# Performance work log

Hardware: AMD Instinct MI355X
Metric: run time of the kernel (lower is better)

The kernel has to match this reference:

```python
import jax, jax.numpy as jnp
import numpy as np

C = 256
POOL = 4

def setup_inputs() -> dict:
    key = jax.random.key(0)
    ks = jax.random.split(key, 8)
    B, H, W = 4, 256, 256
    d = C // 8
    x = jax.random.normal(ks[0], (B, C, H, W), dtype=jnp.float32)
    # 1x1 conv weights stored as [out, in] matrices (kernel_size=1)
    s = 1.0 / np.sqrt(C)
    Wq = jax.random.uniform(ks[1], (d, C), jnp.float32, -s, s)
    bq = jax.random.uniform(ks[2], (d,), jnp.float32, -s, s)
    Wk = jax.random.uniform(ks[3], (d, C), jnp.float32, -s, s)
    bk = jax.random.uniform(ks[4], (d,), jnp.float32, -s, s)
    Wv = jax.random.uniform(ks[5], (C, C), jnp.float32, -s, s)
    bv = jax.random.uniform(ks[6], (C,), jnp.float32, -s, s)
    gamma = jax.random.normal(ks[7], (1,), jnp.float32) * 0.1
    return {"x": x, "Wq": Wq, "bq": bq, "Wk": Wk, "bk": bk,
            "Wv": Wv, "bv": bv, "gamma": gamma}


def reference(x, Wq, bq, Wk, bk, Wv, bv, gamma):
    B, Cc, H, W = x.shape
    Hp, Wp = H // POOL, W // POOL
    # AvgPool2d(kernel=4, stride=4)
    xp = x.reshape(B, Cc, Hp, POOL, Wp, POOL).mean(axis=(3, 5))  # [B,C,Hp,Wp]
    xf = xp.reshape(B, Cc, Hp * Wp)                              # [B,C,N]
    # 1x1 convs == channel matmuls
    q = jnp.einsum('dc,bcn->bdn', Wq, xf) + bq[None, :, None]    # [B,d,N]
    k = jnp.einsum('dc,bcn->bdn', Wk, xf) + bk[None, :, None]    # [B,d,N]
    v = jnp.einsum('ec,bcn->ben', Wv, xf) + bv[None, :, None]    # [B,C,N]
    # energy[b,n,m] = q[:, :, n] . k[:, :, m]
    energy = jnp.einsum('bdn,bdm->bnm', q, k)                    # [B,N,N]
    attn = jax.nn.softmax(energy, axis=-1)
    # out = v @ attn^T  -> out[b,c,n] = sum_m v[b,c,m] * attn[b,n,m]
    out = jnp.einsum('bcm,bnm->bcn', v, attn)                    # [B,C,N]
    out = out.reshape(B, Cc, Hp, Wp)
    # bilinear upsample, half-pixel centers (align_corners=False)
    up = jax.image.resize(out, (B, Cc, H, W), method='bilinear')
    return gamma[0] * up + x
```

## Files before the change

kernel.cpp:

```cpp
#include <hip/hip_runtime.h>

#define B_ 4
#define C_ 256
#define N_ 4096
#define D_ 32

typedef __bf16 bf16;
typedef __bf16 bf16x4 __attribute__((ext_vector_type(4)));
typedef __bf16 bf16x8 __attribute__((ext_vector_type(8)));
typedef float f32x4 __attribute__((ext_vector_type(4)));

__global__ __launch_bounds__(256) void k_prep(
    const float* __restrict__ Wq, const float* __restrict__ bq,
    const float* __restrict__ Wk, const float* __restrict__ bk,
    const float* __restrict__ Wv, const float* __restrict__ bv,
    bf16* __restrict__ wt, float* __restrict__ bias) {
  int r = blockIdx.x, t = threadIdx.x;
  const float* src; float bval;
  if (r < 32)      { src = Wq + (r << 8);        bval = bq[r]; }
  else if (r < 64) { src = Wk + ((r - 32) << 8); bval = bk[r - 32]; }
  else             { src = Wv + ((r - 64) << 8); bval = bv[r - 64]; }
  wt[(r << 8) + t] = (bf16)src[t];
  if (t == 0) bias[r] = bval;
}

__global__ __launch_bounds__(256) void k_fused(const float* __restrict__ x,
    const bf16* __restrict__ wt, const float* __restrict__ bias,
    bf16* __restrict__ qt, bf16* __restrict__ kt, bf16* __restrict__ v) {
  __shared__ bf16 xsb[64][264];
  int tid = threadIdx.x, wave = tid >> 6, l = tid & 63;
  int lg = l >> 4, ll = l & 15;
  int b = blockIdx.x >> 6, hp = blockIdx.x & 63, n0 = hp * 64;

  const float4* x4 = reinterpret_cast<const float4*>(x) +
      ((size_t)((b * 256 + wave * 64) * 256 + hp * 4)) * 64 + l;
  for (int c0 = 0; c0 < 64; c0 += 4) {
    float s[4] = {0.f, 0.f, 0.f, 0.f};
    #pragma unroll
    for (int j = 0; j < 4; ++j) {
      const float4* p = x4 + (size_t)(c0 + j) * 16384;
      #pragma unroll
      for (int dh = 0; dh < 4; ++dh) {
        float4 a = p[dh * 64];
        s[j] += a.x + a.y + a.z + a.w;
      }
    }
    bf16x4 pk;
    #pragma unroll
    for (int j = 0; j < 4; ++j) pk[j] = (bf16)(s[j] * 0.0625f);
    *reinterpret_cast<bf16x4*>(&xsb[l][wave * 64 + c0]) = pk;
  }
  __syncthreads();

  f32x4 acc[5][4];
  #pragma unroll
  for (int j = 0; j < 5; ++j)
    #pragma unroll
    for (int cb = 0; cb < 4; ++cb) acc[j][cb] = (f32x4){0.f, 0.f, 0.f, 0.f};

  for (int kk = 0; kk < 8; ++kk) {
    bf16x8 bfr[4];
    #pragma unroll
    for (int cb = 0; cb < 4; ++cb)
      bfr[cb] = *reinterpret_cast<const bf16x8*>(&xsb[cb * 16 + ll][kk * 32 + lg * 8]);
    #pragma unroll
    for (int j = 0; j < 5; ++j) {
      int rb = wave + j * 4;
      bf16x8 afr = *reinterpret_cast<const bf16x8*>(
          wt + ((size_t)(rb * 16 + ll)) * 256 + kk * 32 + lg * 8);
      #pragma unroll
      for (int cb = 0; cb < 4; ++cb)
        acc[j][cb] = __builtin_amdgcn_mfma_f32_16x16x32_bf16(afr, bfr[cb], acc[j][cb], 0, 0, 0);
    }
  }

  #pragma unroll
  for (int j = 0; j < 5; ++j) {
    int rb = wave + j * 4;
    int row0 = rb * 16 + lg * 4;
    float4 b4 = *reinterpret_cast<const float4*>(bias + row0);
    #pragma unroll
    for (int cb = 0; cb < 4; ++cb) {
      int n = n0 + cb * 16 + ll;
      float v0 = acc[j][cb][0] + b4.x, v1 = acc[j][cb][1] + b4.y;
      float v2 = acc[j][cb][2] + b4.z, v3 = acc[j][cb][3] + b4.w;
      if (row0 < 32) {
        bf16x4 pk = {(bf16)v0, (bf16)v1, (bf16)v2, (bf16)v3};
        *reinterpret_cast<bf16x4*>(qt + ((size_t)(b * N_ + n)) * D_ + row0) = pk;
      } else if (row0 < 64) {
        bf16x4 pk = {(bf16)v0, (bf16)v1, (bf16)v2, (bf16)v3};
        *reinterpret_cast<bf16x4*>(kt + ((size_t)(b * N_ + n)) * D_ + row0 - 32) = pk;
      } else {
        int c = row0 - 64;
        v[((size_t)(b * 256 + c + 0)) * N_ + n] = (bf16)v0;
        v[((size_t)(b * 256 + c + 1)) * N_ + n] = (bf16)v1;
        v[((size_t)(b * 256 + c + 2)) * N_ + n] = (bf16)v2;
        v[((size_t)(b * 256 + c + 3)) * N_ + n] = (bf16)v3;
      }
    }
  }
}

__global__ __launch_bounds__(256) void k_attn(const bf16* __restrict__ qt,
    const bf16* __restrict__ kt, const bf16* __restrict__ v,
    float* __restrict__ outs) {
  __shared__ bf16 p_s[32][264];
  __shared__ float l_stage[4][32];
  __shared__ float l_s[32];
  int tid = threadIdx.x, wave = tid >> 6, l = tid & 63;
  int lg = l >> 4, ll = l & 15;
  int blk = blockIdx.x;
  int b  = (blk & 7) >> 1;
  int nt = ((blk >> 3) << 1) | (blk & 1);
  int n0 = nt * 32;

  const f32x4 fz = {0.f, 0.f, 0.f, 0.f};

  bf16x8 aq[2];
  #pragma unroll
  for (int tnf = 0; tnf < 2; ++tnf)
    aq[tnf] = *reinterpret_cast<const bf16x8*>(
        qt + ((size_t)(b * N_ + n0 + tnf * 16 + ll)) * D_ + lg * 8);

  bf16x8 onesf;
  {
    bf16 o = (bf16)(ll == 0 ? 1.0f : 0.0f);
    #pragma unroll
    for (int e = 0; e < 8; ++e) onesf[e] = o;
  }

  f32x4 acc[2][4];
  f32x4 lacc[2];
  #pragma unroll
  for (int a = 0; a < 2; ++a) {
    lacc[a] = fz;
    #pragma unroll
    for (int cf = 0; cf < 4; ++cf) acc[a][cf] = fz;
  }

  const int mw_off = wave * 64;
  const int cw0    = wave * 64;

  for (int t = 0; t < 16; ++t) {
    int m0 = t * 256;
    #pragma unroll
    for (int tmf = 0; tmf < 4; ++tmf) {
      int mglob = m0 + mw_off + tmf * 16 + ll;
      bf16x8 bk8 = *reinterpret_cast<const bf16x8*>(
          kt + ((size_t)(b * N_ + mglob)) * D_ + lg * 8);
      #pragma unroll
      for (int tnf = 0; tnf < 2; ++tnf) {
        f32x4 e = __builtin_amdgcn_mfma_f32_16x16x32_bf16(aq[tnf], bk8, fz, 0, 0, 0);
        int col = mw_off + tmf * 16 + ll;
        #pragma unroll
        for (int r = 0; r < 4; ++r) {
          float p = __expf(e[r]);
          p_s[tnf * 16 + lg * 4 + r][col] = (bf16)p;
        }
      }
    }
    __syncthreads();
    #pragma unroll
    for (int kk = 0; kk < 8; ++kk) {
      bf16x8 pa[2];
      #pragma unroll
      for (int tnf = 0; tnf < 2; ++tnf)
        pa[tnf] = *reinterpret_cast<const bf16x8*>(
            &p_s[tnf * 16 + ll][kk * 32 + lg * 8]);
      #pragma unroll
      for (int tnf = 0; tnf < 2; ++tnf)
        lacc[tnf] = __builtin_amdgcn_mfma_f32_16x16x32_bf16(pa[tnf], onesf, lacc[tnf], 0, 0, 0);
      #pragma unroll
      for (int cf = 0; cf < 4; ++cf) {
        int c = cw0 + cf * 16 + ll;
        bf16x8 bv8 = *reinterpret_cast<const bf16x8*>(
            v + ((size_t)((b << 8) + c)) * N_ + m0 + kk * 32 + lg * 8);
        acc[0][cf] = __builtin_amdgcn_mfma_f32_16x16x32_bf16(pa[0], bv8, acc[0][cf], 0, 0, 0);
        acc[1][cf] = __builtin_amdgcn_mfma_f32_16x16x32_bf16(pa[1], bv8, acc[1][cf], 0, 0, 0);
      }
    }
    __syncthreads();
  }

  if (ll == 0) {
    #pragma unroll
    for (int tnf = 0; tnf < 2; ++tnf)
      #pragma unroll
      for (int r = 0; r < 4; ++r)
        l_stage[wave][tnf * 16 + lg * 4 + r] = lacc[tnf][r];
  }
  __syncthreads();
  if (tid < 32)
    l_s[tid] = l_stage[0][tid] + l_stage[1][tid] + l_stage[2][tid] + l_stage[3][tid];
  __syncthreads();

  #pragma unroll
  for (int tnf = 0; tnf < 2; ++tnf) {
    #pragma unroll
    for (int r = 0; r < 4; ++r) {
      int tn = tnf * 16 + lg * 4 + r;
      float inv = 1.0f / l_s[tn];
      #pragma unroll
      for (int cf = 0; cf < 4; ++cf) {
        int c = cw0 + cf * 16 + ll;
        outs[((size_t)((b << 8) + c)) * N_ + n0 + tn] = acc[tnf][cf][r] * inv;
      }
    }
  }
}

__global__ __launch_bounds__(256) void k_up(const float* __restrict__ outs,
    const float* __restrict__ x, const float* __restrict__ gamma,
    float* __restrict__ out) {
  int j = blockIdx.x * 256 + threadIdx.x;
  int wq = j & 63, h = (j >> 6) & 255, bc = j >> 14;
  int th = 2 * h - 3;
  int h0 = th < 0 ? -1 : (th >> 3);
  float fh = (float)(th - 8 * h0) * 0.125f;
  int i0h = h0 < 0 ? 0 : h0;
  int i1h = h0 + 1 > 63 ? 63 : h0 + 1;
  const float* s0 = outs + ((size_t)(bc * 64 + i0h)) * 64;
  const float* s1 = outs + ((size_t)(bc * 64 + i1h)) * 64;
  float g = gamma[0];
  float r4[4];
  #pragma unroll
  for (int k2 = 0; k2 < 4; ++k2) {
    int w = wq * 4 + k2;
    int tw = 2 * w - 3;
    int w0 = tw < 0 ? -1 : (tw >> 3);
    float fw = (float)(tw - 8 * w0) * 0.125f;
    int i0 = w0 < 0 ? 0 : w0;
    int i1 = w0 + 1 > 63 ? 63 : w0 + 1;
    float a = s0[i0], bb = s0[i1], cc = s1[i0], dd = s1[i1];
    float top = a + fw * (bb - a);
    float bot = cc + fw * (dd - cc);
    r4[k2] = top + fh * (bot - top);
  }
  size_t o4 = (size_t)(bc * 256 + h) * 64 + wq;
  float4 xv = reinterpret_cast<const float4*>(x)[o4];
  float4 o;
  o.x = g * r4[0] + xv.x; o.y = g * r4[1] + xv.y;
  o.z = g * r4[2] + xv.z; o.w = g * r4[3] + xv.w;
  reinterpret_cast<float4*>(out)[o4] = o;
}

extern "C" void kernel_launch(void* const* d_in, const int* in_sizes, int n_in,
                              void* d_out, int out_size, void* d_ws, size_t ws_size,
                              hipStream_t stream) {
  const float* x     = (const float*)d_in[0];
  const float* Wq    = (const float*)d_in[1];
  const float* bq    = (const float*)d_in[2];
  const float* Wk    = (const float*)d_in[3];
  const float* bk    = (const float*)d_in[4];
  const float* Wv    = (const float*)d_in[5];
  const float* bv    = (const float*)d_in[6];
  const float* gamma = (const float*)d_in[7];
  float* out = (float*)d_out;

  char* ws = (char*)d_ws;
  float* outs = (float*)(ws);
  bf16*  v    = (bf16*) (ws + (16u << 20));
  bf16*  qt   = (bf16*) (ws + (24u << 20));
  bf16*  kt   = (bf16*) (ws + (25u << 20));
  bf16*  wt   = (bf16*) (ws + (26u << 20));
  float* bias = (float*)(ws + (27u << 20));

  hipLaunchKernelGGL(k_prep,  dim3(320),   dim3(256), 0, stream,
                     Wq, bq, Wk, bk, Wv, bv, wt, bias);
  hipLaunchKernelGGL(k_fused, dim3(256),   dim3(256), 0, stream,
                     x, wt, bias, qt, kt, v);
  hipLaunchKernelGGL(k_attn,  dim3(512),   dim3(256), 0, stream, qt, kt, v, outs);
  hipLaunchKernelGGL(k_up,    dim3(65536), dim3(256), 0, stream, outs, x, gamma, out);
}
```

Before: 307.2 us.

## Double threads per block in projection and attention kernels, compute softmax sum in fp32

Both k_fused and k_attn now run 8 waves per block instead of 4, and each wave handles half the channels and keys. This is meant to raise latency hiding with only 256/512 blocks on the device. In k_attn, the row-sum computed by an MFMA against a ones vector is replaced with per-lane fp32 accumulation of exp values followed by shuffle and shared-memory reductions. That removes MFMA work but adds a VALU add per exp. In k_fused, some waves do no work in the last iteration (rb<20), so the load is imbalanced.

After: 298.2 us. -2.9%, faster.

```diff
diff --git a/kernel.cpp b/kernel.cpp
--- a/kernel.cpp
+++ b/kernel.cpp
@@ -24,7 +24,7 @@
   if (t == 0) bias[r] = bval;
 }
 
-__global__ __launch_bounds__(256) void k_fused(const float* __restrict__ x,
+__global__ __launch_bounds__(512) void k_fused(const float* __restrict__ x,
     const bf16* __restrict__ wt, const float* __restrict__ bias,
     bf16* __restrict__ qt, bf16* __restrict__ kt, bf16* __restrict__ v) {
   __shared__ bf16 xsb[64][264];
@@ -33,8 +33,8 @@
   int b = blockIdx.x >> 6, hp = blockIdx.x & 63, n0 = hp * 64;
 
   const float4* x4 = reinterpret_cast<const float4*>(x) +
-      ((size_t)((b * 256 + wave * 64) * 256 + hp * 4)) * 64 + l;
-  for (int c0 = 0; c0 < 64; c0 += 4) {
+      ((size_t)((b * 256 + wave * 32) * 256 + hp * 4)) * 64 + l;
+  for (int c0 = 0; c0 < 32; c0 += 4) {
     float s[4] = {0.f, 0.f, 0.f, 0.f};
     #pragma unroll
     for (int j = 0; j < 4; ++j) {
@@ -48,13 +48,13 @@
     bf16x4 pk;
     #pragma unroll
     for (int j = 0; j < 4; ++j) pk[j] = (bf16)(s[j] * 0.0625f);
-    *reinterpret_cast<bf16x4*>(&xsb[l][wave * 64 + c0]) = pk;
+    *reinterpret_cast<bf16x4*>(&xsb[l][wave * 32 + c0]) = pk;
   }
   __syncthreads();
 
-  f32x4 acc[5][4];
-  #pragma unroll
-  for (int j = 0; j < 5; ++j)
+  f32x4 acc[3][4];
+  #pragma unroll
+  for (int j = 0; j < 3; ++j)
     #pragma unroll
     for (int cb = 0; cb < 4; ++cb) acc[j][cb] = (f32x4){0.f, 0.f, 0.f, 0.f};
 
@@ -64,48 +64,52 @@
     for (int cb = 0; cb < 4; ++cb)
       bfr[cb] = *reinterpret_cast<const bf16x8*>(&xsb[cb * 16 + ll][kk * 32 + lg * 8]);
     #pragma unroll
-    for (int j = 0; j < 5; ++j) {
-      int rb = wave + j * 4;
-      bf16x8 afr = *reinterpret_cast<const bf16x8*>(
-          wt + ((size_t)(rb * 16 + ll)) * 256 + kk * 32 + lg * 8);
-      #pragma unroll
-      for (int cb = 0; cb < 4; ++cb)
-        acc[j][cb] = __builtin_amdgcn_mfma_f32_16x16x32_bf16(afr, bfr[cb], acc[j][cb], 0, 0, 0);
-    }
-  }
-
-  #pragma unroll
-  for (int j = 0; j < 5; ++j) {
-    int rb = wave + j * 4;
-    int row0 = rb * 16 + lg * 4;
-    float4 b4 = *reinterpret_cast<const float4*>(bias + row0);
-    #pragma unroll
-    for (int cb = 0; cb < 4; ++cb) {
-      int n = n0 + cb * 16 + ll;
-      float v0 = acc[j][cb][0] + b4.x, v1 = acc[j][cb][1] + b4.y;
-      float v2 = acc[j][cb][2] + b4.z, v3 = acc[j][cb][3] + b4.w;
-      if (row0 < 32) {
-        bf16x4 pk = {(bf16)v0, (bf16)v1, (bf16)v2, (bf16)v3};
-        *reinterpret_cast<bf16x4*>(qt + ((size_t)(b * N_ + n)) * D_ + row0) = pk;
-      } else if (row0 < 64) {
-        bf16x4 pk = {(bf16)v0, (bf16)v1, (bf16)v2, (bf16)v3};
-        *reinterpret_cast<bf16x4*>(kt + ((size_t)(b * N_ + n)) * D_ + row0 - 32) = pk;
-      } else {
-        int c = row0 - 64;
-        v[((size_t)(b * 256 + c + 0)) * N_ + n] = (bf16)v0;
-        v[((size_t)(b * 256 + c + 1)) * N_ + n] = (bf16)v1;
-        v[((size_t)(b * 256 + c + 2)) * N_ + n] = (bf16)v2;
-        v[((size_t)(b * 256 + c + 3)) * N_ + n] = (bf16)v3;
-      }
-    }
-  }
-}
-
-__global__ __launch_bounds__(256) void k_attn(const bf16* __restrict__ qt,
+    for (int j = 0; j < 3; ++j) {
+      int rb = wave + j * 8;
+      if (rb < 20) {
+        bf16x8 afr = *reinterpret_cast<const bf16x8*>(
+            wt + ((size_t)(rb * 16 + ll)) * 256 + kk * 32 + lg * 8);
+        #pragma unroll
+        for (int cb = 0; cb < 4; ++cb)
+          acc[j][cb] = __builtin_amdgcn_mfma_f32_16x16x32_bf16(afr, bfr[cb], acc[j][cb], 0, 0, 0);
+      }
+    }
+  }
+
+  #pragma unroll
+  for (int j = 0; j < 3; ++j) {
+    int rb = wave + j * 8;
+    if (rb < 20) {
+      int row0 = rb * 16 + lg * 4;
+      float4 b4 = *reinterpret_cast<const float4*>(bias + row0);
+      #pragma unroll
+      for (int cb = 0; cb < 4; ++cb) {
+        int n = n0 + cb * 16 + ll;
+        float v0 = acc[j][cb][0] + b4.x, v1 = acc[j][cb][1] + b4.y;
+        float v2 = acc[j][cb][2] + b4.z, v3 = acc[j][cb][3] + b4.w;
+        if (row0 < 32) {
+          bf16x4 pk = {(bf16)v0, (bf16)v1, (bf16)v2, (bf16)v3};
+          *reinterpret_cast<bf16x4*>(qt + ((size_t)(b * N_ + n)) * D_ + row0) = pk;
+        } else if (row0 < 64) {
+          bf16x4 pk = {(bf16)v0, (bf16)v1, (bf16)v2, (bf16)v3};
+          *reinterpret_cast<bf16x4*>(kt + ((size_t)(b * N_ + n)) * D_ + row0 - 32) = pk;
+        } else {
+          int c = row0 - 64;
+          v[((size_t)(b * 256 + c + 0)) * N_ + n] = (bf16)v0;
+          v[((size_t)(b * 256 + c + 1)) * N_ + n] = (bf16)v1;
+          v[((size_t)(b * 256 + c + 2)) * N_ + n] = (bf16)v2;
+          v[((size_t)(b * 256 + c + 3)) * N_ + n] = (bf16)v3;
+        }
+      }
+    }
+  }
+}
+
+__global__ __launch_bounds__(512) void k_attn(const bf16* __restrict__ qt,
     const bf16* __restrict__ kt, const bf16* __restrict__ v,
     float* __restrict__ outs) {
   __shared__ bf16 p_s[32][264];
-  __shared__ float l_stage[4][32];
+  __shared__ float l_red[8][32];
   __shared__ float l_s[32];
   int tid = threadIdx.x, wave = tid >> 6, l = tid & 63;
   int lg = l >> 4, ll = l & 15;
@@ -122,39 +126,34 @@
     aq[tnf] = *reinterpret_cast<const bf16x8*>(
         qt + ((size_t)(b * N_ + n0 + tnf * 16 + ll)) * D_ + lg * 8);
 
-  bf16x8 onesf;
-  {
-    bf16 o = (bf16)(ll == 0 ? 1.0f : 0.0f);
-    #pragma unroll
-    for (int e = 0; e < 8; ++e) onesf[e] = o;
-  }
-
-  f32x4 acc[2][4];
-  f32x4 lacc[2];
+  f32x4 acc[2][2];
+  float lsum[2][4];
   #pragma unroll
   for (int a = 0; a < 2; ++a) {
-    lacc[a] = fz;
-    #pragma unroll
-    for (int cf = 0; cf < 4; ++cf) acc[a][cf] = fz;
-  }
-
-  const int mw_off = wave * 64;
-  const int cw0    = wave * 64;
+    #pragma unroll
+    for (int cf = 0; cf < 2; ++cf) acc[a][cf] = fz;
+    #pragma unroll
+    for (int r = 0; r < 4; ++r) lsum[a][r] = 0.f;
+  }
+
+  const int mw = wave * 32;
+  const int cw = wave * 32;
 
   for (int t = 0; t < 16; ++t) {
     int m0 = t * 256;
     #pragma unroll
-    for (int tmf = 0; tmf < 4; ++tmf) {
-      int mglob = m0 + mw_off + tmf * 16 + ll;
+    for (int tmf = 0; tmf < 2; ++tmf) {
+      int mglob = m0 + mw + tmf * 16 + ll;
       bf16x8 bk8 = *reinterpret_cast<const bf16x8*>(
           kt + ((size_t)(b * N_ + mglob)) * D_ + lg * 8);
       #pragma unroll
       for (int tnf = 0; tnf < 2; ++tnf) {
         f32x4 e = __builtin_amdgcn_mfma_f32_16x16x32_bf16(aq[tnf], bk8, fz, 0, 0, 0);
-        int col = mw_off + tmf * 16 + ll;
+        int col = mw + tmf * 16 + ll;
         #pragma unroll
         for (int r = 0; r < 4; ++r) {
           float p = __expf(e[r]);
+          lsum[tnf][r] += p;
           p_s[tnf * 16 + lg * 4 + r][col] = (bf16)p;
         }
       }
@@ -168,11 +167,8 @@
         pa[tnf] = *reinterpret_cast<const bf16x8*>(
             &p_s[tnf * 16 + ll][kk * 32 + lg * 8]);
       #pragma unroll
-      for (int tnf = 0; tnf < 2; ++tnf)
-        lacc[tnf] = __builtin_amdgcn_mfma_f32_16x16x32_bf16(pa[tnf], onesf, lacc[tnf], 0, 0, 0);
-      #pragma unroll
-      for (int cf = 0; cf < 4; ++cf) {
-        int c = cw0 + cf * 16 + ll;
+      for (int cf = 0; cf < 2; ++cf) {
+        int c = cw + cf * 16 + ll;
         bf16x8 bv8 = *reinterpret_cast<const bf16x8*>(
             v + ((size_t)((b << 8) + c)) * N_ + m0 + kk * 32 + lg * 8);
         acc[0][cf] = __builtin_amdgcn_mfma_f32_16x16x32_bf16(pa[0], bv8, acc[0][cf], 0, 0, 0);
@@ -182,16 +178,25 @@
     __syncthreads();
   }
 
-  if (ll == 0) {
-    #pragma unroll
-    for (int tnf = 0; tnf < 2; ++tnf)
-      #pragma unroll
-      for (int r = 0; r < 4; ++r)
-        l_stage[wave][tnf * 16 + lg * 4 + r] = lacc[tnf][r];
+  #pragma unroll
+  for (int tnf = 0; tnf < 2; ++tnf) {
+    #pragma unroll
+    for (int r = 0; r < 4; ++r) {
+      float s = lsum[tnf][r];
+      s += __shfl_xor(s, 1);
+      s += __shfl_xor(s, 2);
+      s += __shfl_xor(s, 4);
+      s += __shfl_xor(s, 8);
+      if (ll == 0) l_red[wave][tnf * 16 + lg * 4 + r] = s;
+    }
   }
   __syncthreads();
-  if (tid < 32)
-    l_s[tid] = l_stage[0][tid] + l_stage[1][tid] + l_stage[2][tid] + l_stage[3][tid];
+  if (tid < 32) {
+    float s = 0.f;
+    #pragma unroll
+    for (int w = 0; w < 8; ++w) s += l_red[w][tid];
+    l_s[tid] = s;
+  }
   __syncthreads();
 
   #pragma unroll
@@ -201,8 +206,8 @@
       int tn = tnf * 16 + lg * 4 + r;
       float inv = 1.0f / l_s[tn];
       #pragma unroll
-      for (int cf = 0; cf < 4; ++cf) {
-        int c = cw0 + cf * 16 + ll;
+      for (int cf = 0; cf < 2; ++cf) {
+        int c = cw + cf * 16 + ll;
         outs[((size_t)((b << 8) + c)) * N_ + n0 + tn] = acc[tnf][cf][r] * inv;
       }
     }
@@ -267,8 +272,8 @@
 
   hipLaunchKernelGGL(k_prep,  dim3(320),   dim3(256), 0, stream,
                      Wq, bq, Wk, bk, Wv, bv, wt, bias);
-  hipLaunchKernelGGL(k_fused, dim3(256),   dim3(256), 0, stream,
+  hipLaunchKernelGGL(k_fused, dim3(256),   dim3(512), 0, stream,
                      x, wt, bias, qt, kt, v);
-  hipLaunchKernelGGL(k_attn,  dim3(512),   dim3(256), 0, stream, qt, kt, v, outs);
+  hipLaunchKernelGGL(k_attn,  dim3(512),   dim3(512), 0, stream, qt, kt, v, outs);
   hipLaunchKernelGGL(k_up,    dim3(65536), dim3(256), 0, stream, outs, x, gamma, out);
 }
```
